# Optimization experiments

Hardware: AMD Instinct MI355X
Metric: run time of the kernel (lower is better)

## Reference

```python
import jax, jax.numpy as jnp
import numpy as np

B, H, M_DIM, K, N = 4, 8, 2048, 2048, 64
NNZ = B * H * M_DIM * 64


def setup_inputs() -> dict:
    key = jax.random.key(0)
    k_val, k_b, k_bh, k_m, k_k = jax.random.split(key, 5)
    values = jax.random.normal(k_val, (NNZ,), dtype=jnp.float32)
    b = jax.random.normal(k_b, (B, H, K, N), dtype=jnp.float32)
    idx_bh = jax.random.randint(k_bh, (NNZ,), 0, B * H, dtype=jnp.int32)
    idx_m = jax.random.randint(k_m, (NNZ,), 0, M_DIM, dtype=jnp.int32)
    idx_k = jax.random.randint(k_k, (NNZ,), 0, K, dtype=jnp.int32)
    return {"values": values, "b": b, "idx_bh": idx_bh, "idx_m": idx_m,
            "idx_k": idx_k, "M": M_DIM}


def reference(values, b, idx_bh, idx_m, idx_k, M):
    # Batched sparse-dense matmul: out[b,h,m,:] = sum_k A[b,h,m,k] * b[b,h,k,:]
    # A is in COO form over flattened batch-head dim: (idx_bh, idx_m, idx_k, values).
    Bd, Hd, Kd, Nd = b.shape
    b_flat = b.reshape(Bd * Hd, Kd, Nd)             # [BH, K, N]
    # gather the dense rows each nonzero touches, scale by the sparse value
    gathered = values[:, None] * b_flat[idx_bh, idx_k]  # [nnz, N]
    # scatter-add into output rows (flat segment id = bh*M + m)
    seg = idx_bh * M + idx_m
    out = jax.ops.segment_sum(gathered, seg, num_segments=Bd * Hd * M)  # [BH*M, N]
    return out.reshape(Bd, Hd, M, Nd)
```

## Files before the change

kernel.cpp:

```cpp
#include <hip/hip_runtime.h>

constexpr int N_COLS = 64;
constexpr int K_DIM  = 2048;
constexpr int M_DIM  = 2048;
constexpr int SEGS   = 32 * 2048;
constexpr int NBUCK  = 512;
constexpr int SEG_PER_BUCK = SEGS / NBUCK;
constexpr int PART_T = 512;
constexpr int PART_E = 16;
constexpr int TILE   = PART_T * PART_E;
constexpr int CAP    = 8960;
constexpr int CSTR   = 16;

struct Pair { float v; int k; };

__global__ void spmm_coo_atomic(const float* __restrict__ values,
                                const float* __restrict__ b,
                                const int*   __restrict__ idx_bh,
                                const int*   __restrict__ idx_m,
                                const int*   __restrict__ idx_k,
                                float*       __restrict__ out,
                                int nnz) {
    long long gid = (long long)blockIdx.x * blockDim.x + threadIdx.x;
    int nz   = (int)(gid >> 6);
    int lane = (int)(gid & 63);
    if (nz >= nnz) return;
    float bval = b[((size_t)idx_bh[nz] * K_DIM + idx_k[nz]) * N_COLS + lane];
    atomicAdd(&out[((size_t)idx_bh[nz] * M_DIM + idx_m[nz]) * N_COLS + lane],
              values[nz] * bval);
}

__global__ void hist512(const int* __restrict__ idx_bh,
                        const int* __restrict__ idx_m,
                        int* __restrict__ counts, int nnz) {
    __shared__ int h[NBUCK];
    int t = threadIdx.x;
    h[t] = 0;
    __syncthreads();
    int base = blockIdx.x * TILE;
    for (int i = 0; i < PART_E; ++i) {
        int e = base + t + i * PART_T;
        if (e < nnz) {
            int seg = idx_bh[e] * M_DIM + idx_m[e];
            atomicAdd(&h[seg >> 7], 1);
        }
    }
    __syncthreads();
    if (h[t] > 0) atomicAdd(&counts[t * CSTR], h[t]);
}

__global__ void scan512(int* __restrict__ cursor, int* __restrict__ boff) {
    __shared__ int s[NBUCK];
    int t = threadIdx.x;
    int c = cursor[t * CSTR];
    s[t] = c;
    __syncthreads();
    for (int d = 1; d < NBUCK; d <<= 1) {
        int x = (t >= d) ? s[t - d] : 0;
        __syncthreads();
        s[t] += x;
        __syncthreads();
    }
    int excl = s[t] - c;
    boff[t]        = excl;
    cursor[t*CSTR] = excl;
    if (t == NBUCK - 1) boff[NBUCK] = s[t];
}

__global__ __launch_bounds__(PART_T)
void partition512(const float* __restrict__ values,
                  const int*   __restrict__ idx_bh,
                  const int*   __restrict__ idx_m,
                  const int*   __restrict__ idx_k,
                  int*  __restrict__ cursor,
                  Pair* __restrict__ packed, int nnz, int cap) {
    __shared__ int lcount[NBUCK];
    __shared__ int lbase[NBUCK];
    int t = threadIdx.x;
    lcount[t] = 0;
    __syncthreads();

    int e0 = blockIdx.x * TILE + t * PART_E;
    float v[PART_E];
    int   pk[PART_E];
    short bkt[PART_E];
    short rnk[PART_E];

    if (e0 + PART_E <= nnz) {
        const float4* vv4 = (const float4*)(values + e0);
        const int4*   bh4 = (const int4*)(idx_bh + e0);
        const int4*   mm4 = (const int4*)(idx_m + e0);
        const int4*   kk4 = (const int4*)(idx_k + e0);
        #pragma unroll
        for (int q = 0; q < PART_E / 4; ++q) {
            float4 vq = vv4[q];
            int4   bq = bh4[q], mq = mm4[q], kq = kk4[q];
            int s0 = bq.x * M_DIM + mq.x;
            int s1 = bq.y * M_DIM + mq.y;
            int s2 = bq.z * M_DIM + mq.z;
            int s3 = bq.w * M_DIM + mq.w;
            v[4*q+0]=vq.x; pk[4*q+0]=(kq.x<<8)|((s0&127)<<19); bkt[4*q+0]=(short)(s0>>7);
            rnk[4*q+0]=(short)atomicAdd(&lcount[s0>>7],1);
            v[4*q+1]=vq.y; pk[4*q+1]=(kq.y<<8)|((s1&127)<<19); bkt[4*q+1]=(short)(s1>>7);
            rnk[4*q+1]=(short)atomicAdd(&lcount[s1>>7],1);
            v[4*q+2]=vq.z; pk[4*q+2]=(kq.z<<8)|((s2&127)<<19); bkt[4*q+2]=(short)(s2>>7);
            rnk[4*q+2]=(short)atomicAdd(&lcount[s2>>7],1);
            v[4*q+3]=vq.w; pk[4*q+3]=(kq.w<<8)|((s3&127)<<19); bkt[4*q+3]=(short)(s3>>7);
            rnk[4*q+3]=(short)atomicAdd(&lcount[s3>>7],1);
        }
    } else {
        #pragma unroll
        for (int i = 0; i < PART_E; ++i) {
            int e = e0 + i;
            if (e < nnz) {
                int seg = idx_bh[e] * M_DIM + idx_m[e];
                int bu  = seg >> 7;
                v[i]  = values[e];
                pk[i] = (idx_k[e] << 8) | ((seg & 127) << 19);
                bkt[i] = (short)bu;
                rnk[i] = (short)atomicAdd(&lcount[bu], 1);
            } else bkt[i] = -1;
        }
    }
    __syncthreads();
    int c = lcount[t];
    lbase[t] = t * cap + ((c > 0) ? atomicAdd(&cursor[t * CSTR], c) : 0);
    __syncthreads();
    #pragma unroll
    for (int i = 0; i < PART_E; ++i) {
        if (bkt[i] >= 0) {
            Pair p; p.v = v[i]; p.k = pk[i];
            packed[lbase[bkt[i]] + rnk[i]] = p;
        }
    }
}

__global__ __launch_bounds__(1024)
void sort_accum(const Pair* __restrict__ packed,
                const int*  __restrict__ cursor,
                const int*  __restrict__ boff,
                const float* __restrict__ b,
                float* __restrict__ out, int cap) {
    __shared__ int2 ps[CAP + 8];
    __shared__ int h[SEG_PER_BUCK];
    __shared__ int cur[SEG_PER_BUCK];

    int t = threadIdx.x;
    int i   = blockIdx.x;
    int bkt = (i & 7) * 64 + (i >> 3);
    int start, L;
    if (cap) { start = bkt * cap;  L = cursor[bkt * CSTR]; }
    else     { start = boff[bkt];  L = boff[bkt + 1] - start; }
    if (L < 0)   L = 0;
    if (L > CAP) L = CAP;

    if (t < SEG_PER_BUCK) h[t] = 0;
    if (t < 8) ps[L + t] = make_int2(0, 0);
    __syncthreads();

    const int2* src = (const int2*)(packed + start);
    int2 reg[9];
    #pragma unroll
    for (int q = 0; q < 9; ++q) {
        int idx = t + q * 1024;
        if (idx < L) {
            reg[q] = src[idx];
            atomicAdd(&h[(reg[q].y >> 19) & 127], 1);
        }
    }
    __syncthreads();

    for (int d = 1; d < SEG_PER_BUCK; d <<= 1) {
        int x = 0;
        if (t < SEG_PER_BUCK && t >= d) x = h[t - d];
        __syncthreads();
        if (t < SEG_PER_BUCK && t >= d) h[t] += x;
        __syncthreads();
    }
    if (t < SEG_PER_BUCK) cur[t] = (t == 0) ? 0 : h[t - 1];
    __syncthreads();

    #pragma unroll
    for (int q = 0; q < 9; ++q) {
        int idx = t + q * 1024;
        if (idx < L) {
            int pos = atomicAdd(&cur[(reg[q].y >> 19) & 127], 1);
            ps[pos] = make_int2(reg[q].y & 0x0007FF00, reg[q].x);
        }
    }
    __syncthreads();

    int lane = t & 63;
    int w    = t >> 6;
    int bh   = bkt >> 4;
    const char* bbyte = (const char*)(b + ((size_t)bh << 17));
    size_t obase = ((size_t)bkt << 13);

    for (int s = w * 8; s < w * 8 + 8; ++s) {
        int js = (s == 0) ? 0 : h[s - 1];
        int je = h[s];
        float a0 = 0.f, a1 = 0.f, a2 = 0.f, a3 = 0.f;
        int j = js;
        for (; j + 8 <= je; j += 8) {
            int2 e0 = ps[j+0], e1 = ps[j+1], e2 = ps[j+2], e3 = ps[j+3];
            int2 e4 = ps[j+4], e5 = ps[j+5], e6 = ps[j+6], e7 = ps[j+7];
            const float* r0 = (const float*)(bbyte + __builtin_amdgcn_readfirstlane(e0.x));
            const float* r1 = (const float*)(bbyte + __builtin_amdgcn_readfirstlane(e1.x));
            const float* r2 = (const float*)(bbyte + __builtin_amdgcn_readfirstlane(e2.x));
            const float* r3 = (const float*)(bbyte + __builtin_amdgcn_readfirstlane(e3.x));
            const float* r4 = (const float*)(bbyte + __builtin_amdgcn_readfirstlane(e4.x));
            const float* r5 = (const float*)(bbyte + __builtin_amdgcn_readfirstlane(e5.x));
            const float* r6 = (const float*)(bbyte + __builtin_amdgcn_readfirstlane(e6.x));
            const float* r7 = (const float*)(bbyte + __builtin_amdgcn_readfirstlane(e7.x));
            float b0 = r0[lane], b1 = r1[lane], b2 = r2[lane], b3 = r3[lane];
            float b4 = r4[lane], b5 = r5[lane], b6 = r6[lane], b7 = r7[lane];
            a0 += __int_as_float(e0.y) * b0; a1 += __int_as_float(e1.y) * b1;
            a2 += __int_as_float(e2.y) * b2; a3 += __int_as_float(e3.y) * b3;
            a0 += __int_as_float(e4.y) * b4; a1 += __int_as_float(e5.y) * b5;
            a2 += __int_as_float(e6.y) * b6; a3 += __int_as_float(e7.y) * b7;
        }
        if (j < je) {
            int2 e0 = ps[j+0], e1 = ps[j+1], e2 = ps[j+2], e3 = ps[j+3];
            int2 e4 = ps[j+4], e5 = ps[j+5], e6 = ps[j+6], e7 = ps[j+7];
            const float* r0 = (const float*)(bbyte + __builtin_amdgcn_readfirstlane(e0.x));
            const float* r1 = (const float*)(bbyte + __builtin_amdgcn_readfirstlane(e1.x));
            const float* r2 = (const float*)(bbyte + __builtin_amdgcn_readfirstlane(e2.x));
            const float* r3 = (const float*)(bbyte + __builtin_amdgcn_readfirstlane(e3.x));
            const float* r4 = (const float*)(bbyte + __builtin_amdgcn_readfirstlane(e4.x));
            const float* r5 = (const float*)(bbyte + __builtin_amdgcn_readfirstlane(e5.x));
            const float* r6 = (const float*)(bbyte + __builtin_amdgcn_readfirstlane(e6.x));
            const float* r7 = (const float*)(bbyte + __builtin_amdgcn_readfirstlane(e7.x));
            float b0 = r0[lane], b1 = r1[lane], b2 = r2[lane], b3 = r3[lane];
            float b4 = r4[lane], b5 = r5[lane], b6 = r6[lane], b7 = r7[lane];
            float v0 = (j+0 < je) ? __int_as_float(e0.y) : 0.f;
            float v1 = (j+1 < je) ? __int_as_float(e1.y) : 0.f;
            float v2 = (j+2 < je) ? __int_as_float(e2.y) : 0.f;
            float v3 = (j+3 < je) ? __int_as_float(e3.y) : 0.f;
            float v4 = (j+4 < je) ? __int_as_float(e4.y) : 0.f;
            float v5 = (j+5 < je) ? __int_as_float(e5.y) : 0.f;
            float v6 = (j+6 < je) ? __int_as_float(e6.y) : 0.f;
            float v7 = (j+7 < je) ? __int_as_float(e7.y) : 0.f;
            a0 += v0 * b0; a1 += v1 * b1; a2 += v2 * b2; a3 += v3 * b3;
            a0 += v4 * b4; a1 += v5 * b5; a2 += v6 * b6; a3 += v7 * b7;
        }
        out[obase + ((size_t)s << 6) + lane] = (a0 + a1) + (a2 + a3);
    }
}

extern "C" void kernel_launch(void* const* d_in, const int* in_sizes, int n_in,
                              void* d_out, int out_size, void* d_ws, size_t ws_size,
                              hipStream_t stream) {
    const float* values = (const float*)d_in[0];
    const float* b      = (const float*)d_in[1];
    const int*   idx_bh = (const int*)d_in[2];
    const int*   idx_m  = (const int*)d_in[3];
    const int*   idx_k  = (const int*)d_in[4];
    float*       out    = (float*)d_out;
    const int    nnz    = in_sizes[0];

    const size_t packed_off = 512 * 1024;
    const size_t dense_sz   = (size_t)nnz * sizeof(Pair);
    const size_t fc_sz      = (size_t)NBUCK * CAP * sizeof(Pair);
    const size_t need_fc    = packed_off + fc_sz;
    const size_t need_dense = packed_off + dense_sz;

    int*  cursor = (int*)d_ws;
    int*  boff   = (int*)((char*)d_ws + 32768);
    Pair* packed = (Pair*)((char*)d_ws + packed_off);

    const int nblk = (nnz + TILE - 1) / TILE;

    if (ws_size >= need_fc) {
        hipMemsetAsync(cursor, 0, NBUCK * CSTR * sizeof(int), stream);
        partition512<<<nblk, PART_T, 0, stream>>>(values, idx_bh, idx_m, idx_k,
                                                  cursor, packed, nnz, CAP);
        sort_accum<<<NBUCK, 1024, 0, stream>>>(packed, cursor, boff, b, out, CAP);
    } else if (ws_size >= need_dense) {
        hipMemsetAsync(cursor, 0, NBUCK * CSTR * sizeof(int), stream);
        hist512<<<nblk, PART_T, 0, stream>>>(idx_bh, idx_m, cursor, nnz);
        scan512<<<1, NBUCK, 0, stream>>>(cursor, boff);
        partition512<<<nblk, PART_T, 0, stream>>>(values, idx_bh, idx_m, idx_k,
                                                  cursor, packed, nnz, 0);
        sort_accum<<<NBUCK, 1024, 0, stream>>>(packed, cursor, boff, b, out, 0);
    } else {
        hipMemsetAsync(d_out, 0, (size_t)out_size * sizeof(float), stream);
        long long total = (long long)nnz * N_COLS;
        spmm_coo_atomic<<<(unsigned)((total + 255) / 256), 256, 0, stream>>>(
            values, b, idx_bh, idx_m, idx_k, out, nnz);
    }
}
```

Before: 197.1 us.

## Shrink per-bucket capacity and add global overflow buffer for spill entries

```diff
diff --git a/kernel.cpp b/kernel.cpp
--- a/kernel.cpp
+++ b/kernel.cpp
@@ -9,8 +9,12 @@
 constexpr int PART_T = 512;
 constexpr int PART_E = 16;
 constexpr int TILE   = PART_T * PART_E;
-constexpr int CAP    = 8960;
+constexpr int CAP2   = 8192;
 constexpr int CSTR   = 16;
+constexpr int OVL_CAP = 640;
+constexpr size_t OVFCNT_OFF = 32768;
+constexpr size_t OVFBUF_OFF = 40960;
+constexpr int OVF_GCAP = (int)((524288 - OVFBUF_OFF) / 8);
 
 struct Pair { float v; int k; };
 
@@ -30,52 +34,17 @@
               values[nz] * bval);
 }
 
-__global__ void hist512(const int* __restrict__ idx_bh,
-                        const int* __restrict__ idx_m,
-                        int* __restrict__ counts, int nnz) {
-    __shared__ int h[NBUCK];
-    int t = threadIdx.x;
-    h[t] = 0;
-    __syncthreads();
-    int base = blockIdx.x * TILE;
-    for (int i = 0; i < PART_E; ++i) {
-        int e = base + t + i * PART_T;
-        if (e < nnz) {
-            int seg = idx_bh[e] * M_DIM + idx_m[e];
-            atomicAdd(&h[seg >> 7], 1);
-        }
-    }
-    __syncthreads();
-    if (h[t] > 0) atomicAdd(&counts[t * CSTR], h[t]);
-}
-
-__global__ void scan512(int* __restrict__ cursor, int* __restrict__ boff) {
-    __shared__ int s[NBUCK];
-    int t = threadIdx.x;
-    int c = cursor[t * CSTR];
-    s[t] = c;
-    __syncthreads();
-    for (int d = 1; d < NBUCK; d <<= 1) {
-        int x = (t >= d) ? s[t - d] : 0;
-        __syncthreads();
-        s[t] += x;
-        __syncthreads();
-    }
-    int excl = s[t] - c;
-    boff[t]        = excl;
-    cursor[t*CSTR] = excl;
-    if (t == NBUCK - 1) boff[NBUCK] = s[t];
-}
-
 __global__ __launch_bounds__(PART_T)
 void partition512(const float* __restrict__ values,
                   const int*   __restrict__ idx_bh,
                   const int*   __restrict__ idx_m,
                   const int*   __restrict__ idx_k,
                   int*  __restrict__ cursor,
-                  Pair* __restrict__ packed, int nnz, int cap) {
+                  int*  __restrict__ ovfcnt,
+                  Pair* __restrict__ ovf,
+                  Pair* __restrict__ packed, int nnz) {
     __shared__ int lcount[NBUCK];
-    __shared__ int lbase[NBUCK];
+    __shared__ int sbase[NBUCK];
     int t = threadIdx.x;
     lcount[t] = 0;
     __syncthreads();
@@ -124,13 +93,23 @@
     }
     __syncthreads();
     int c = lcount[t];
-    lbase[t] = t * cap + ((c > 0) ? atomicAdd(&cursor[t * CSTR], c) : 0);
+    sbase[t] = (c > 0) ? atomicAdd(&cursor[t * CSTR], c) : 0;
     __syncthreads();
     #pragma unroll
     for (int i = 0; i < PART_E; ++i) {
         if (bkt[i] >= 0) {
-            Pair p; p.v = v[i]; p.k = pk[i];
-            packed[lbase[bkt[i]] + rnk[i]] = p;
+            int g = sbase[bkt[i]] + rnk[i];
+            Pair p; p.v = v[i];
+            if (g < CAP2) {
+                p.k = pk[i];
+                packed[(size_t)bkt[i] * CAP2 + g] = p;
+            } else {
+                int o = atomicAdd(ovfcnt, 1);
+                if (o < OVF_GCAP) {
+                    p.k = pk[i] | ((int)bkt[i] & 0xFF) | ((((int)bkt[i]) >> 8) << 26);
+                    ovf[o] = p;
+                }
+            }
         }
     }
 }
@@ -138,34 +117,50 @@
 __global__ __launch_bounds__(1024)
 void sort_accum(const Pair* __restrict__ packed,
                 const int*  __restrict__ cursor,
-                const int*  __restrict__ boff,
+                const int*  __restrict__ ovfcnt,
+                const Pair* __restrict__ ovf,
                 const float* __restrict__ b,
-                float* __restrict__ out, int cap) {
-    __shared__ int2 ps[CAP + 8];
+                float* __restrict__ out) {
+    __shared__ int2 ps[CAP2 + OVL_CAP + 8];
+    __shared__ int2 ovl[OVL_CAP];
     __shared__ int h[SEG_PER_BUCK];
     __shared__ int cur[SEG_PER_BUCK];
+    __shared__ int ovl_n;
 
     int t = threadIdx.x;
     int i   = blockIdx.x;
     int bkt = (i & 7) * 64 + (i >> 3);
-    int start, L;
-    if (cap) { start = bkt * cap;  L = cursor[bkt * CSTR]; }
-    else     { start = boff[bkt];  L = boff[bkt + 1] - start; }
-    if (L < 0)   L = 0;
-    if (L > CAP) L = CAP;
+    int cnt = cursor[bkt * CSTR];
+    int L = cnt;
+    if (L < 0)    L = 0;
+    if (L > CAP2) L = CAP2;
 
     if (t < SEG_PER_BUCK) h[t] = 0;
-    if (t < 8) ps[L + t] = make_int2(0, 0);
-    __syncthreads();
-
-    const int2* src = (const int2*)(packed + start);
-    int2 reg[9];
+    if (t == 0) ovl_n = 0;
+    __syncthreads();
+
+    const int2* src = (const int2*)(packed + (size_t)bkt * CAP2);
+    int2 reg[8];
     #pragma unroll
-    for (int q = 0; q < 9; ++q) {
+    for (int q = 0; q < 8; ++q) {
         int idx = t + q * 1024;
         if (idx < L) {
             reg[q] = src[idx];
             atomicAdd(&h[(reg[q].y >> 19) & 127], 1);
+        }
+    }
+    int ovfN = ovfcnt[0];
+    if (ovfN > OVF_GCAP) ovfN = OVF_GCAP;
+    const int2* osrc = (const int2*)ovf;
+    for (int o = t; o < ovfN; o += 1024) {
+        int2 e = osrc[o];
+        int eb = (e.y & 0xFF) | ((e.y >> 18) & 0x100);
+        if (eb == bkt) {
+            int pos = atomicAdd(&ovl_n, 1);
+            if (pos < OVL_CAP) {
+                ovl[pos] = e;
+                atomicAdd(&h[(e.y >> 19) & 127], 1);
+            }
         }
     }
     __syncthreads();
@@ -181,13 +176,21 @@
     __syncthreads();
 
     #pragma unroll
-    for (int q = 0; q < 9; ++q) {
+    for (int q = 0; q < 8; ++q) {
         int idx = t + q * 1024;
         if (idx < L) {
             int pos = atomicAdd(&cur[(reg[q].y >> 19) & 127], 1);
             ps[pos] = make_int2(reg[q].y & 0x0007FF00, reg[q].x);
         }
     }
+    int on = ovl_n; if (on > OVL_CAP) on = OVL_CAP;
+    if (t < on) {
+        int2 e = ovl[t];
+        int pos = atomicAdd(&cur[(e.y >> 19) & 127], 1);
+        ps[pos] = make_int2(e.y & 0x0007FF00, e.x);
+    }
+    __syncthreads();
+    if (t < 8) ps[h[SEG_PER_BUCK - 1] + t] = make_int2(0, 0);
     __syncthreads();
 
     int lane = t & 63;
@@ -259,29 +262,20 @@
     const int    nnz    = in_sizes[0];
 
     const size_t packed_off = 512 * 1024;
-    const size_t dense_sz   = (size_t)nnz * sizeof(Pair);
-    const size_t fc_sz      = (size_t)NBUCK * CAP * sizeof(Pair);
-    const size_t need_fc    = packed_off + fc_sz;
-    const size_t need_dense = packed_off + dense_sz;
+    const size_t need = packed_off + (size_t)NBUCK * CAP2 * sizeof(Pair);
 
     int*  cursor = (int*)d_ws;
-    int*  boff   = (int*)((char*)d_ws + 32768);
+    int*  ovfcnt = (int*)((char*)d_ws + OVFCNT_OFF);
+    Pair* ovfbuf = (Pair*)((char*)d_ws + OVFBUF_OFF);
     Pair* packed = (Pair*)((char*)d_ws + packed_off);
 
     const int nblk = (nnz + TILE - 1) / TILE;
 
-    if (ws_size >= need_fc) {
-        hipMemsetAsync(cursor, 0, NBUCK * CSTR * sizeof(int), stream);
+    if (ws_size >= need) {
+        hipMemsetAsync(d_ws, 0, OVFBUF_OFF, stream);
         partition512<<<nblk, PART_T, 0, stream>>>(values, idx_bh, idx_m, idx_k,
-                                                  cursor, packed, nnz, CAP);
-        sort_accum<<<NBUCK, 1024, 0, stream>>>(packed, cursor, boff, b, out, CAP);
-    } else if (ws_size >= need_dense) {
-        hipMemsetAsync(cursor, 0, NBUCK * CSTR * sizeof(int), stream);
-        hist512<<<nblk, PART_T, 0, stream>>>(idx_bh, idx_m, cursor, nnz);
-        scan512<<<1, NBUCK, 0, stream>>>(cursor, boff);
-        partition512<<<nblk, PART_T, 0, stream>>>(values, idx_bh, idx_m, idx_k,
-                                                  cursor, packed, nnz, 0);
-        sort_accum<<<NBUCK, 1024, 0, stream>>>(packed, cursor, boff, b, out, 0);
+                                                  cursor, ovfcnt, ovfbuf, packed, nnz);
+        sort_accum<<<NBUCK, 1024, 0, stream>>>(packed, cursor, ovfcnt, ovfbuf, b, out);
     } else {
         hipMemsetAsync(d_out, 0, (size_t)out_size * sizeof(float), stream);
         long long total = (long long)nnz * N_COLS;
```

After: 224.1 us. +13.7%, slower.
